# Kernel optimization log

Hardware: AMD Instinct MI355X
Metric: run time of the kernel (lower is better)

Reference implementation:

```python
import jax, jax.numpy as jnp
import numpy as np

N = 12288
D = 256
GAMMA = 0.5
NEG_INF = jnp.float32(-9.0e15)


def setup_inputs() -> dict:
    key = jax.random.key(0)
    k1, k2, k3, k4, k5, k6, k7 = jax.random.split(key, 7)
    h_eu = jax.random.normal(k1, (N, D), dtype=jnp.float32)
    h_po = jax.random.normal(k2, (N, D), dtype=jnp.float32)
    h_lo = jax.random.normal(k3, (N, D), dtype=jnp.float32)
    u = jax.random.uniform(k4, (N, N), dtype=jnp.float32)
    adj = jnp.where(u > 0.9, u, jnp.float32(0.0))
    xav = np.sqrt(2.0) * np.sqrt(6.0 / (D + 1))  # xavier_uniform gain sqrt(2)
    a1 = jax.random.uniform(k5, (D, 1), dtype=jnp.float32, minval=-xav, maxval=xav)
    a2 = jax.random.uniform(k6, (D, 1), dtype=jnp.float32, minval=-xav, maxval=xav)
    a3 = jax.random.uniform(k7, (D, 1), dtype=jnp.float32, minval=-xav, maxval=xav)
    return {"h_eu": h_eu, "h_po": h_po, "h_lo": h_lo, "adj": adj,
            "a1": a1, "a2": a2, "a3": a3}


def reference(h_eu, h_po, h_lo, adj, a1, a2, a3):
    # rank-1 outer-sum score matrix: e[i,j] = <h_eu[i],a1> + <h_po[j],a2> + <h_lo[i],a3>
    e_eu = h_eu @ a1                      # (N,1)
    e_po = (h_po @ a2).T                  # (1,N)
    e_lo = h_lo @ a3                      # (N,1)
    e = jax.nn.leaky_relu(e_eu + e_po + e_lo)  # (N,N), slope 0.01 as in torch
    att = jnp.where(adj > 0, e, NEG_INF)
    att = jax.nn.softmax(att, axis=1)
    # scale each row i by degree (row-sum) of adj row i
    att = att * jnp.sum(adj, axis=1, keepdims=True)
    att = GAMMA * att + (1.0 - GAMMA) * adj
    return att @ h_po                     # (N,D)
```

## Files before the change

kernel.cpp:

```cpp
#include <hip/hip_runtime.h>
#include <hip/hip_bf16.h>


#define NN 12288
#define DD 256
#define BM 48
#define BK 64
#define NSTEPS (NN / BK)
#define BOFF 12288
#define VOFF 45056
#define BUFSZ 45312
#define LOG2E 1.44269504f
#define SHIFT2 36.067376f

typedef __attribute__((ext_vector_type(8))) short s16x8;
typedef __attribute__((ext_vector_type(4))) float f32x4;

__device__ __forceinline__ unsigned short f2bf(float f) {
  unsigned u = __builtin_bit_cast(unsigned, f);
  u += 0x7FFFu + ((u >> 16) & 1u);
  return (unsigned short)(u >> 16);
}
__device__ __forceinline__ unsigned pack_bf2(float a, float b) {
  unsigned short lo = __builtin_bit_cast(unsigned short, __float2bfloat16(a));
  unsigned short hi = __builtin_bit_cast(unsigned short, __float2bfloat16(b));
  return (unsigned)lo | ((unsigned)hi << 16);
}
__device__ __forceinline__ float exp2_hw(float x) {
  float r;
  asm("v_exp_f32 %0, %1" : "=v"(r) : "v"(x));
  return r;
}
__device__ __forceinline__ void gl_lds16(const void* g, void* l) {
  __builtin_amdgcn_global_load_lds(
      (const __attribute__((address_space(1))) void*)g,
      (__attribute__((address_space(3))) void*)l, 16, 0, 0);
}
__device__ __forceinline__ void gl_lds4(const void* g, void* l) {
  __builtin_amdgcn_global_load_lds(
      (const __attribute__((address_space(1))) void*)g,
      (__attribute__((address_space(3))) void*)l, 4, 0, 0);
}

__global__ __launch_bounds__(256) void prep_uv(
    const float* __restrict__ h_eu, const float* __restrict__ h_po,
    const float* __restrict__ h_lo, const float* __restrict__ a1,
    const float* __restrict__ a2, const float* __restrict__ a3,
    float* __restrict__ u, float* __restrict__ v) {
  const int t = threadIdx.x;
  const int wave = t >> 6, lane = t & 63;
  const int r0 = blockIdx.x * 64;
  for (int rr = 0; rr < 16; ++rr) {
    const int row = r0 + wave * 16 + rr;
    const float* pe = h_eu + (size_t)row * DD;
    const float* pl = h_lo + (size_t)row * DD;
    const float* pp = h_po + (size_t)row * DD;
    float su = 0.f, sv = 0.f;
#pragma unroll
    for (int c = 0; c < 4; ++c) {
      const int d = lane + c * 64;
      su = fmaf(pe[d], a1[d], su);
      su = fmaf(pl[d], a3[d], su);
      sv = fmaf(pp[d], a2[d], sv);
    }
#pragma unroll
    for (int m = 32; m; m >>= 1) {
      su += __shfl_xor(su, m, 64);
      sv += __shfl_xor(sv, m, 64);
    }
    if (lane == 0) { u[row] = su * LOG2E; v[row] = sv * LOG2E; }
  }
}

__global__ __launch_bounds__(256) void prep_T(
    const float* __restrict__ hpo, unsigned short* __restrict__ h_poT) {
  const int t = threadIdx.x;
  const int r0 = blockIdx.x * 64;
  unsigned short* dst = h_poT + (size_t)t * NN + r0;
#pragma unroll
  for (int c = 0; c < 16; ++c) {
    unsigned short x0 = f2bf(hpo[(size_t)(r0 + c * 4 + 0) * DD + t]);
    unsigned short x1 = f2bf(hpo[(size_t)(r0 + c * 4 + 1) * DD + t]);
    unsigned short x2 = f2bf(hpo[(size_t)(r0 + c * 4 + 2) * DD + t]);
    unsigned short x3 = f2bf(hpo[(size_t)(r0 + c * 4 + 3) * DD + t]);
    ((uint2*)dst)[c] = make_uint2((unsigned)x0 | ((unsigned)x1 << 16),
                                  (unsigned)x2 | ((unsigned)x3 << 16));
  }
}

__global__ __launch_bounds__(1024) void fused13(
    const float* __restrict__ adj, const float* __restrict__ u2,
    const float* __restrict__ v2, const unsigned short* __restrict__ h_poT,
    float* __restrict__ out) {
  __shared__ __align__(16) char sMem[3 * BUFSZ];
  __shared__ float sq[2][3][16], sa[2][3][16];

  const int t = threadIdx.x;
  const int w = t >> 6, lane = t & 63;
  const int lrow = lane & 15, kgrp = lane >> 4;
  const int i0 = blockIdx.x * BM;

  if (w < 12) {
    const int rg = w >> 2;
    const int dh = (w >> 1) & 1;
    const int kh = w & 1;
    const int row = i0 + rg * 16 + lrow;
    const float u_r = u2[row];
    const float uc1 = u_r - SHIFT2;
    const float uc2 = fmaf(0.01f, u_r, -SHIFT2);
    const int xr = (lrow & 7) << 4;

    const int aOff = (rg * 16 + lrow) * 256;
    const int kA0 = (kh * 128 + kgrp * 32) ^ xr;
    const int kA1 = (kh * 128 + kgrp * 32 + 16) ^ xr;
    const int bOff = BOFF + (dh * 128 + lrow) * 128 + ((kh * 64 + kgrp * 16) ^ xr);
    const int vOff = VOFF + (kh * 32 + kgrp * 8) * 4;

    f32x4 acc1[8] = {};
    f32x4 acc2[8] = {};
    float qsum = 0.f, asum = 0.f;

    __syncthreads();

    int buf = 0;
    for (int s = 0; s < NSTEPS; ++s) {
      const char* bufp = sMem + buf * BUFSZ;
      const f32x4 Vv0 = *(const f32x4*)(bufp + vOff);
      const f32x4 Vv1 = *(const f32x4*)(bufp + vOff + 16);
      const char* ab = bufp + aOff;
      const f32x4 A0 = *(const f32x4*)(ab + kA0);
      const f32x4 A1 = *(const f32x4*)(ab + kA1);
      const float af[8] = {A0[0], A0[1], A0[2], A0[3],
                           A1[0], A1[1], A1[2], A1[3]};
      const float vf[8] = {Vv0[0], Vv0[1], Vv0[2], Vv0[3],
                           Vv1[0], Vv1[1], Vv1[2], Vv1[3]};
      float qv[8];
#pragma unroll
      for (int e = 0; e < 8; ++e) {
        const float t1 = uc1 + vf[e];
        const float t2 = fmaf(0.01f, vf[e], uc2);
        float q = exp2_hw(fmaxf(t1, t2));
        q = (af[e] > 0.f) ? q : 0.f;
        qsum += q; asum += af[e]; qv[e] = q;
      }
      unsigned qp[4], ap[4];
#pragma unroll
      for (int e = 0; e < 4; ++e) {
        qp[e] = pack_bf2(qv[2 * e], qv[2 * e + 1]);
        ap[e] = pack_bf2(af[2 * e], af[2 * e + 1]);
      }
      const s16x8 qa = __builtin_bit_cast(s16x8, *(uint4*)qp);
      const s16x8 aa = __builtin_bit_cast(s16x8, *(uint4*)ap);
      const char* bb = bufp + bOff;
#pragma unroll
      for (int dt = 0; dt < 8; ++dt) {
        const s16x8 b = *(const s16x8*)(bb + dt * 2048);
        acc1[dt] = __builtin_amdgcn_mfma_f32_16x16x32_bf16(qa, b, acc1[dt], 0, 0, 0);
        acc2[dt] = __builtin_amdgcn_mfma_f32_16x16x32_bf16(aa, b, acc2[dt], 0, 0, 0);
      }
      __syncthreads();
      buf = (buf == 2) ? 0 : buf + 1;
    }

    qsum += __shfl_xor(qsum, 16, 64); qsum += __shfl_xor(qsum, 32, 64);
    asum += __shfl_xor(asum, 16, 64); asum += __shfl_xor(asum, 32, 64);
    if (dh == 0 && lane < 16) { sq[kh][rg][lane] = qsum; sa[kh][rg][lane] = asum; }
    __syncthreads();

    f32x4 fin[8];
#pragma unroll
    for (int dt = 0; dt < 8; ++dt) {
#pragma unroll
      for (int g = 0; g < 4; ++g) {
        const int rr = kgrp * 4 + g;
        const float qq = sq[0][rg][rr] + sq[1][rg][rr];
        const float aa2 = sa[0][rg][rr] + sa[1][rg][rr];
        const float cfr = qq > 0.f ? 0.5f * aa2 / qq : 0.f;
        fin[dt][g] = cfr * acc1[dt][g] + 0.5f * acc2[dt][g];
      }
    }
    float* red = (float*)sMem;
    const int rbase = ((rg * 2 + dh) * 8 * 64 + lane) * 4;
    if (kh == 1) {
#pragma unroll
      for (int dt = 0; dt < 8; ++dt) *(f32x4*)&red[rbase + dt * 256] = fin[dt];
    }
    __syncthreads();
    if (kh == 0) {
#pragma unroll
      for (int dt = 0; dt < 8; ++dt) {
        const f32x4 o = *(const f32x4*)&red[rbase + dt * 256];
        const int col = dh * 128 + dt * 16 + lrow;
#pragma unroll
        for (int g = 0; g < 4; ++g)
          out[(size_t)(i0 + rg * 16 + kgrp * 4 + g) * DD + col] = fin[dt][g] + o[g];
      }
    }
  } else {
    const int pid = w - 12;
    const char* pA[3];
    int dA[3];
#pragma unroll
    for (int j = 0; j < 3; ++j) {
      const int idx = pid * 3 + j;
      pA[j] = (const char*)(adj + (size_t)(i0 + idx * 4 + (lane >> 4)) * NN)
              + (((lane & 15) ^ ((idx & 1) * 4 + (lane >> 4))) << 4);
      dA[j] = idx * 1024;
    }
    const int ko = ((lane & 7) ^ (lane >> 3)) << 4;
    const char* pB[8];
    int dB[8];
#pragma unroll
    for (int j = 0; j < 8; ++j) {
      const int ib = pid * 8 + j;
      pB[j] = (const char*)h_poT + (size_t)(ib * 8 + (lane >> 3)) * (NN * 2) + ko;
      dB[j] = BOFF + ib * 1024;
    }
    const float* pV = v2 + lane;

#pragma unroll
    for (int b = 0; b < 2; ++b) {
      char* nb = sMem + b * BUFSZ;
#pragma unroll
      for (int j = 0; j < 3; ++j) { gl_lds16(pA[j], nb + dA[j]); pA[j] += 256; }
#pragma unroll
      for (int j = 0; j < 8; ++j) { gl_lds16(pB[j], nb + dB[j]); pB[j] += 128; }
      gl_lds4(pV, nb + VOFF); pV += 64;
    }
    asm volatile("s_waitcnt vmcnt(12)" ::: "memory");
    __builtin_amdgcn_s_barrier();

    int nbuf = 2;
    for (int s = 0; s < NSTEPS; ++s) {
      if (s < NSTEPS - 2) {
        char* nb = sMem + nbuf * BUFSZ;
#pragma unroll
        for (int j = 0; j < 3; ++j) { gl_lds16(pA[j], nb + dA[j]); pA[j] += 256; }
#pragma unroll
        for (int j = 0; j < 8; ++j) { gl_lds16(pB[j], nb + dB[j]); pB[j] += 128; }
        gl_lds4(pV, nb + VOFF); pV += 64;
        asm volatile("s_waitcnt vmcnt(12)" ::: "memory");
      } else if (s == NSTEPS - 2) {
        asm volatile("s_waitcnt vmcnt(0)" ::: "memory");
      }
      __builtin_amdgcn_s_barrier();
      nbuf = (nbuf == 2) ? 0 : nbuf + 1;
    }
    __syncthreads();
    __syncthreads();
  }
}

__global__ __launch_bounds__(256) void fused_fb(
    const float* __restrict__ adj, const float* __restrict__ u,
    const float* __restrict__ v, const float* __restrict__ hpo,
    float* __restrict__ out) {
#define BMF 32
#define LDA 40
  __shared__ unsigned short qlds[BMF][LDA];
  __shared__ unsigned short alds[BMF][LDA];
  __shared__ unsigned short btf[DD][LDA];
  __shared__ float denom_s[BMF], deg_s[BMF], coef_s[BMF];

  const int t = threadIdx.x;
  const int wave = t >> 6, lane = t & 63;
  const int i0 = blockIdx.x * BMF;
  const int sr = t >> 3;
  const int sc = (t & 7) * 4;
  const float u_r = u[i0 + sr];
  const int d0 = wave * 64;
  const int lrow = lane & 15;
  const int kgrp = lane >> 4;

  f32x4 acc1[2][4] = {};
  f32x4 acc2[2][4] = {};
  float qsum = 0.f, asum = 0.f;

  const float* arow = adj + (size_t)(i0 + sr) * NN + sc;
  float4 a_cur = *(const float4*)(arow);

  constexpr int NSTEP = NN / 32;
  for (int jt = 0; jt < NSTEP; ++jt) {
    const int j = jt * 32;
    float4 a_nxt;
    const bool has_next = (jt + 1 < NSTEP);
    if (has_next) a_nxt = *(const float4*)(arow + j + 32);
    const float4 vv = *(const float4*)(v + j + sc);
    unsigned short qb[4], ab[4];
    {
      const float aa4[4] = {a_cur.x, a_cur.y, a_cur.z, a_cur.w};
      const float vvv[4] = {vv.x, vv.y, vv.z, vv.w};
#pragma unroll
      for (int k = 0; k < 4; ++k) {
        const float a = aa4[k];
        const float s = u_r + vvv[k];
        const float x = fmaxf(s, 0.01f * s);
        const float q = (a > 0.f) ? exp2_hw(x - SHIFT2) : 0.f;
        qsum += q;
        asum += a;
        qb[k] = f2bf(q);
        ab[k] = f2bf(a);
      }
    }
    *(uint2*)&qlds[sr][sc] = make_uint2((unsigned)qb[0] | ((unsigned)qb[1] << 16),
                                        (unsigned)qb[2] | ((unsigned)qb[3] << 16));
    *(uint2*)&alds[sr][sc] = make_uint2((unsigned)ab[0] | ((unsigned)ab[1] << 16),
                                        (unsigned)ab[2] | ((unsigned)ab[3] << 16));
    {
      const int br = t >> 3;
      const float* src = hpo + (size_t)(j + br) * DD;
#pragma unroll
      for (int cc = 0; cc < 8; ++cc) {
        const int c = (t & 7) * 4 + cc * 32;
        const float4 hv = *(const float4*)(src + c);
        btf[c + 0][br] = f2bf(hv.x);
        btf[c + 1][br] = f2bf(hv.y);
        btf[c + 2][br] = f2bf(hv.z);
        btf[c + 3][br] = f2bf(hv.w);
      }
    }
    __syncthreads();

    const s16x8 qa0 = *(const s16x8*)&qlds[lrow][kgrp * 8];
    const s16x8 qa1 = *(const s16x8*)&qlds[16 + lrow][kgrp * 8];
    const s16x8 ad0 = *(const s16x8*)&alds[lrow][kgrp * 8];
    const s16x8 ad1 = *(const s16x8*)&alds[16 + lrow][kgrp * 8];
#pragma unroll
    for (int dt = 0; dt < 4; ++dt) {
      const s16x8 b = *(const s16x8*)&btf[d0 + dt * 16 + lrow][kgrp * 8];
      acc1[0][dt] = __builtin_amdgcn_mfma_f32_16x16x32_bf16(qa0, b, acc1[0][dt], 0, 0, 0);
      acc1[1][dt] = __builtin_amdgcn_mfma_f32_16x16x32_bf16(qa1, b, acc1[1][dt], 0, 0, 0);
      acc2[0][dt] = __builtin_amdgcn_mfma_f32_16x16x32_bf16(ad0, b, acc2[0][dt], 0, 0, 0);
      acc2[1][dt] = __builtin_amdgcn_mfma_f32_16x16x32_bf16(ad1, b, acc2[1][dt], 0, 0, 0);
    }
    __syncthreads();
    if (has_next) a_cur = a_nxt;
  }
#pragma unroll
  for (int m = 1; m <= 4; m <<= 1) {
    qsum += __shfl_xor(qsum, m, 64);
    asum += __shfl_xor(asum, m, 64);
  }
  if ((t & 7) == 0) { denom_s[sr] = qsum; deg_s[sr] = asum; }
  __syncthreads();
  if (t < BMF) {
    const float dn = denom_s[t];
    coef_s[t] = dn > 0.f ? 0.5f * deg_s[t] / dn : 0.f;
  }
  __syncthreads();
#pragma unroll
  for (int f = 0; f < 2; ++f) {
#pragma unroll
    for (int dt = 0; dt < 4; ++dt) {
      const int col = d0 + dt * 16 + lrow;
#pragma unroll
      for (int g = 0; g < 4; ++g) {
        const int r = f * 16 + kgrp * 4 + g;
        out[(size_t)(i0 + r) * DD + col] =
            coef_s[r] * acc1[f][dt][g] + 0.5f * acc2[f][dt][g];
      }
    }
  }
}

extern "C" void kernel_launch(void* const* d_in, const int* in_sizes, int n_in,
                              void* d_out, int out_size, void* d_ws, size_t ws_size,
                              hipStream_t stream) {
  const float* h_eu = (const float*)d_in[0];
  const float* h_po = (const float*)d_in[1];
  const float* h_lo = (const float*)d_in[2];
  const float* adj  = (const float*)d_in[3];
  const float* a1   = (const float*)d_in[4];
  const float* a2   = (const float*)d_in[5];
  const float* a3   = (const float*)d_in[6];
  float* out = (float*)d_out;

  const size_t need_full = (size_t)2 * NN * 4 + (size_t)NN * DD * 2;
  float* u = (float*)d_ws;
  float* v = u + NN;
  unsigned short* h_poT = (unsigned short*)(v + NN);
  const bool big_ws = ws_size >= need_full;

  prep_uv<<<NN / 64, 256, 0, stream>>>(h_eu, h_po, h_lo, a1, a2, a3, u, v);
  if (big_ws) {
    prep_T<<<NN / 64, 256, 0, stream>>>(h_po, h_poT);
    fused13<<<NN / BM, 1024, 0, stream>>>(adj, u, v, h_poT, out);
  } else {
    fused_fb<<<NN / 32, 256, 0, stream>>>(adj, u, v, h_po, out);
  }
}
```

Before: 253.3 us.

## Load h_poT B-operand directly from global into registers instead of LDS staging

Compute warps now read the transposed bf16 h_po tile straight from global memory into registers each k-step, and the producer warps only stage adjacency and v into shared memory. This shrinks the per-stage LDS buffer and removes LDS write/read traffic for B. In exchange, B is fetched redundantly by the three row-group warps and without software prefetch, so global/L2 latency lands directly in the MFMA loop.

Result: slower. 667.4 us (+163.5%).

```diff
diff --git a/kernel.cpp b/kernel.cpp
--- a/kernel.cpp
+++ b/kernel.cpp
@@ -7,9 +7,8 @@
 #define BM 48
 #define BK 64
 #define NSTEPS (NN / BK)
-#define BOFF 12288
-#define VOFF 45056
-#define BUFSZ 45312
+#define VOFF 12288
+#define BUFSZ 12544
 #define LOG2E 1.44269504f
 #define SHIFT2 36.067376f
 
@@ -88,11 +87,11 @@
   }
 }
 
-__global__ __launch_bounds__(1024) void fused13(
+__global__ __launch_bounds__(1024) void fused14(
     const float* __restrict__ adj, const float* __restrict__ u2,
     const float* __restrict__ v2, const unsigned short* __restrict__ h_poT,
     float* __restrict__ out) {
-  __shared__ __align__(16) char sMem[3 * BUFSZ];
+  __shared__ __align__(16) char sMem[49152];
   __shared__ float sq[2][3][16], sa[2][3][16];
 
   const int t = threadIdx.x;
@@ -113,8 +112,13 @@
     const int aOff = (rg * 16 + lrow) * 256;
     const int kA0 = (kh * 128 + kgrp * 32) ^ xr;
     const int kA1 = (kh * 128 + kgrp * 32 + 16) ^ xr;
-    const int bOff = BOFF + (dh * 128 + lrow) * 128 + ((kh * 64 + kgrp * 16) ^ xr);
     const int vOff = VOFF + (kh * 32 + kgrp * 8) * 4;
+
+    const char* bbase[8];
+#pragma unroll
+    for (int dt = 0; dt < 8; ++dt)
+      bbase[dt] = (const char*)h_poT + (size_t)(dh * 128 + dt * 16) * (NN * 2);
+    unsigned boff = (unsigned)(lrow * NN + kh * 32 + kgrp * 8) * 2;
 
     f32x4 acc1[8] = {};
     f32x4 acc2[8] = {};
@@ -124,6 +128,12 @@
 
     int buf = 0;
     for (int s = 0; s < NSTEPS; ++s) {
+      uint4 b[8];
+#pragma unroll
+      for (int dt = 0; dt < 8; ++dt)
+        b[dt] = *(const uint4*)(bbase[dt] + boff);
+      boff += 128;
+
       const char* bufp = sMem + buf * BUFSZ;
       const f32x4 Vv0 = *(const f32x4*)(bufp + vOff);
       const f32x4 Vv1 = *(const f32x4*)(bufp + vOff + 16);
@@ -151,12 +161,11 @@
       }
       const s16x8 qa = __builtin_bit_cast(s16x8, *(uint4*)qp);
       const s16x8 aa = __builtin_bit_cast(s16x8, *(uint4*)ap);
-      const char* bb = bufp + bOff;
 #pragma unroll
       for (int dt = 0; dt < 8; ++dt) {
-        const s16x8 b = *(const s16x8*)(bb + dt * 2048);
-        acc1[dt] = __builtin_amdgcn_mfma_f32_16x16x32_bf16(qa, b, acc1[dt], 0, 0, 0);
-        acc2[dt] = __builtin_amdgcn_mfma_f32_16x16x32_bf16(aa, b, acc2[dt], 0, 0, 0);
+        const s16x8 bb = __builtin_bit_cast(s16x8, b[dt]);
+        acc1[dt] = __builtin_amdgcn_mfma_f32_16x16x32_bf16(qa, bb, acc1[dt], 0, 0, 0);
+        acc2[dt] = __builtin_amdgcn_mfma_f32_16x16x32_bf16(aa, bb, acc2[dt], 0, 0, 0);
       }
       __syncthreads();
       buf = (buf == 2) ? 0 : buf + 1;
@@ -207,15 +216,6 @@
               + (((lane & 15) ^ ((idx & 1) * 4 + (lane >> 4))) << 4);
       dA[j] = idx * 1024;
     }
-    const int ko = ((lane & 7) ^ (lane >> 3)) << 4;
-    const char* pB[8];
-    int dB[8];
-#pragma unroll
-    for (int j = 0; j < 8; ++j) {
-      const int ib = pid * 8 + j;
-      pB[j] = (const char*)h_poT + (size_t)(ib * 8 + (lane >> 3)) * (NN * 2) + ko;
-      dB[j] = BOFF + ib * 1024;
-    }
     const float* pV = v2 + lane;
 
 #pragma unroll
@@ -223,11 +223,9 @@
       char* nb = sMem + b * BUFSZ;
 #pragma unroll
       for (int j = 0; j < 3; ++j) { gl_lds16(pA[j], nb + dA[j]); pA[j] += 256; }
-#pragma unroll
-      for (int j = 0; j < 8; ++j) { gl_lds16(pB[j], nb + dB[j]); pB[j] += 128; }
       gl_lds4(pV, nb + VOFF); pV += 64;
     }
-    asm volatile("s_waitcnt vmcnt(12)" ::: "memory");
+    asm volatile("s_waitcnt vmcnt(4)" ::: "memory");
     __builtin_amdgcn_s_barrier();
 
     int nbuf = 2;
@@ -236,10 +234,8 @@
         char* nb = sMem + nbuf * BUFSZ;
 #pragma unroll
         for (int j = 0; j < 3; ++j) { gl_lds16(pA[j], nb + dA[j]); pA[j] += 256; }
-#pragma unroll
-        for (int j = 0; j < 8; ++j) { gl_lds16(pB[j], nb + dB[j]); pB[j] += 128; }
         gl_lds4(pV, nb + VOFF); pV += 64;
-        asm volatile("s_waitcnt vmcnt(12)" ::: "memory");
+        asm volatile("s_waitcnt vmcnt(4)" ::: "memory");
       } else if (s == NSTEPS - 2) {
         asm volatile("s_waitcnt vmcnt(0)" ::: "memory");
       }
@@ -384,7 +380,7 @@
   prep_uv<<<NN / 64, 256, 0, stream>>>(h_eu, h_po, h_lo, a1, a2, a3, u, v);
   if (big_ws) {
     prep_T<<<NN / 64, 256, 0, stream>>>(h_po, h_poT);
-    fused13<<<NN / BM, 1024, 0, stream>>>(adj, u, v, h_poT, out);
+    fused14<<<NN / BM, 1024, 0, stream>>>(adj, u, v, h_poT, out);
   } else {
     fused_fb<<<NN / 32, 256, 0, stream>>>(adj, u, v, h_po, out);
   }
```

## Cut compute waves to four, each covering three row groups, two blocks per CU

Applied to the files above, without the earlier changes.

Compute warps drop from 12 to 4. Each one now handles all three 16-row groups, so every B fragment loaded from LDS feeds three times as many MFMAs and B reads from LDS fall. The block shrinks from 1024 to 512 threads with launch bounds (512,2), aiming for two resident blocks per CU. The cost is six times the accumulator registers per compute thread (48 f32x4 instead of 16). That risks spilling, and with fewer compute waves there is less latency hiding for the exp and packing work.

New measurement: 522.2 us. +106.2%, slower.

```diff
diff --git a/kernel.cpp b/kernel.cpp
--- a/kernel.cpp
+++ b/kernel.cpp
@@ -88,7 +88,7 @@
   }
 }
 
-__global__ __launch_bounds__(1024) void fused13(
+__global__ __launch_bounds__(512, 2) void fused15(
     const float* __restrict__ adj, const float* __restrict__ u2,
     const float* __restrict__ v2, const unsigned short* __restrict__ h_poT,
     float* __restrict__ out) {
@@ -100,25 +100,28 @@
   const int lrow = lane & 15, kgrp = lane >> 4;
   const int i0 = blockIdx.x * BM;
 
-  if (w < 12) {
-    const int rg = w >> 2;
-    const int dh = (w >> 1) & 1;
+  if (w < 4) {
+    const int dh = w >> 1;
     const int kh = w & 1;
-    const int row = i0 + rg * 16 + lrow;
-    const float u_r = u2[row];
-    const float uc1 = u_r - SHIFT2;
-    const float uc2 = fmaf(0.01f, u_r, -SHIFT2);
     const int xr = (lrow & 7) << 4;
 
-    const int aOff = (rg * 16 + lrow) * 256;
+    float uc1[3], uc2[3];
+#pragma unroll
+    for (int m = 0; m < 3; ++m) {
+      const float ur = u2[i0 + m * 16 + lrow];
+      uc1[m] = ur - SHIFT2;
+      uc2[m] = fmaf(0.01f, ur, -SHIFT2);
+    }
+
+    const int aOff0 = lrow * 256;
     const int kA0 = (kh * 128 + kgrp * 32) ^ xr;
     const int kA1 = (kh * 128 + kgrp * 32 + 16) ^ xr;
     const int bOff = BOFF + (dh * 128 + lrow) * 128 + ((kh * 64 + kgrp * 16) ^ xr);
     const int vOff = VOFF + (kh * 32 + kgrp * 8) * 4;
 
-    f32x4 acc1[8] = {};
-    f32x4 acc2[8] = {};
-    float qsum = 0.f, asum = 0.f;
+    f32x4 acc1[3][8] = {};
+    f32x4 acc2[3][8] = {};
+    float qsum[3] = {0.f, 0.f, 0.f}, asum[3] = {0.f, 0.f, 0.f};
 
     __syncthreads();
 
@@ -127,77 +130,107 @@
       const char* bufp = sMem + buf * BUFSZ;
       const f32x4 Vv0 = *(const f32x4*)(bufp + vOff);
       const f32x4 Vv1 = *(const f32x4*)(bufp + vOff + 16);
-      const char* ab = bufp + aOff;
-      const f32x4 A0 = *(const f32x4*)(ab + kA0);
-      const f32x4 A1 = *(const f32x4*)(ab + kA1);
-      const float af[8] = {A0[0], A0[1], A0[2], A0[3],
-                           A1[0], A1[1], A1[2], A1[3]};
       const float vf[8] = {Vv0[0], Vv0[1], Vv0[2], Vv0[3],
                            Vv1[0], Vv1[1], Vv1[2], Vv1[3]};
-      float qv[8];
-#pragma unroll
-      for (int e = 0; e < 8; ++e) {
-        const float t1 = uc1 + vf[e];
-        const float t2 = fmaf(0.01f, vf[e], uc2);
-        float q = exp2_hw(fmaxf(t1, t2));
-        q = (af[e] > 0.f) ? q : 0.f;
-        qsum += q; asum += af[e]; qv[e] = q;
-      }
-      unsigned qp[4], ap[4];
-#pragma unroll
-      for (int e = 0; e < 4; ++e) {
-        qp[e] = pack_bf2(qv[2 * e], qv[2 * e + 1]);
-        ap[e] = pack_bf2(af[2 * e], af[2 * e + 1]);
-      }
-      const s16x8 qa = __builtin_bit_cast(s16x8, *(uint4*)qp);
-      const s16x8 aa = __builtin_bit_cast(s16x8, *(uint4*)ap);
+
+      s16x8 qa[3], aa[3];
+#pragma unroll
+      for (int m = 0; m < 3; ++m) {
+        const char* ab = bufp + aOff0 + m * 4096;
+        const f32x4 A0 = *(const f32x4*)(ab + kA0);
+        const f32x4 A1 = *(const f32x4*)(ab + kA1);
+        const float af[8] = {A0[0], A0[1], A0[2], A0[3],
+                             A1[0], A1[1], A1[2], A1[3]};
+        float qv[8];
+#pragma unroll
+        for (int e = 0; e < 8; ++e) {
+          const float t1 = uc1[m] + vf[e];
+          const float t2 = fmaf(0.01f, vf[e], uc2[m]);
+          float q = exp2_hw(fmaxf(t1, t2));
+          q = (af[e] > 0.f) ? q : 0.f;
+          qsum[m] += q; asum[m] += af[e]; qv[e] = q;
+        }
+        unsigned qp[4], ap[4];
+#pragma unroll
+        for (int e = 0; e < 4; ++e) {
+          qp[e] = pack_bf2(qv[2 * e], qv[2 * e + 1]);
+          ap[e] = pack_bf2(af[2 * e], af[2 * e + 1]);
+        }
+        qa[m] = __builtin_bit_cast(s16x8, *(uint4*)qp);
+        aa[m] = __builtin_bit_cast(s16x8, *(uint4*)ap);
+      }
+
       const char* bb = bufp + bOff;
 #pragma unroll
       for (int dt = 0; dt < 8; ++dt) {
         const s16x8 b = *(const s16x8*)(bb + dt * 2048);
-        acc1[dt] = __builtin_amdgcn_mfma_f32_16x16x32_bf16(qa, b, acc1[dt], 0, 0, 0);
-        acc2[dt] = __builtin_amdgcn_mfma_f32_16x16x32_bf16(aa, b, acc2[dt], 0, 0, 0);
+#pragma unroll
+        for (int m = 0; m < 3; ++m) {
+          acc1[m][dt] = __builtin_amdgcn_mfma_f32_16x16x32_bf16(qa[m], b, acc1[m][dt], 0, 0, 0);
+          acc2[m][dt] = __builtin_amdgcn_mfma_f32_16x16x32_bf16(aa[m], b, acc2[m][dt], 0, 0, 0);
+        }
       }
       __syncthreads();
       buf = (buf == 2) ? 0 : buf + 1;
     }
 
-    qsum += __shfl_xor(qsum, 16, 64); qsum += __shfl_xor(qsum, 32, 64);
-    asum += __shfl_xor(asum, 16, 64); asum += __shfl_xor(asum, 32, 64);
-    if (dh == 0 && lane < 16) { sq[kh][rg][lane] = qsum; sa[kh][rg][lane] = asum; }
-    __syncthreads();
-
-    f32x4 fin[8];
-#pragma unroll
-    for (int dt = 0; dt < 8; ++dt) {
-#pragma unroll
-      for (int g = 0; g < 4; ++g) {
-        const int rr = kgrp * 4 + g;
-        const float qq = sq[0][rg][rr] + sq[1][rg][rr];
-        const float aa2 = sa[0][rg][rr] + sa[1][rg][rr];
-        const float cfr = qq > 0.f ? 0.5f * aa2 / qq : 0.f;
-        fin[dt][g] = cfr * acc1[dt][g] + 0.5f * acc2[dt][g];
-      }
-    }
+#pragma unroll
+    for (int m = 0; m < 3; ++m) {
+      qsum[m] += __shfl_xor(qsum[m], 16, 64);
+      qsum[m] += __shfl_xor(qsum[m], 32, 64);
+      asum[m] += __shfl_xor(asum[m], 16, 64);
+      asum[m] += __shfl_xor(asum[m], 32, 64);
+    }
+    if (dh == 0 && lane < 16) {
+#pragma unroll
+      for (int m = 0; m < 3; ++m) {
+        sq[kh][m][lane] = qsum[m];
+        sa[kh][m][lane] = asum[m];
+      }
+    }
+    __syncthreads();
+
     float* red = (float*)sMem;
-    const int rbase = ((rg * 2 + dh) * 8 * 64 + lane) * 4;
     if (kh == 1) {
 #pragma unroll
-      for (int dt = 0; dt < 8; ++dt) *(f32x4*)&red[rbase + dt * 256] = fin[dt];
+      for (int m = 0; m < 3; ++m) {
+#pragma unroll
+        for (int dt = 0; dt < 8; ++dt) {
+          f32x4 fin;
+#pragma unroll
+          for (int g = 0; g < 4; ++g) {
+            const int rr = kgrp * 4 + g;
+            const float qq = sq[0][m][rr] + sq[1][m][rr];
+            const float aa2 = sa[0][m][rr] + sa[1][m][rr];
+            const float cfr = qq > 0.f ? 0.5f * aa2 / qq : 0.f;
+            fin[g] = cfr * acc1[m][dt][g] + 0.5f * acc2[m][dt][g];
+          }
+          *(f32x4*)&red[(((dh * 3 + m) * 8 + dt) * 64 + lane) * 4] = fin;
+        }
+      }
     }
     __syncthreads();
     if (kh == 0) {
 #pragma unroll
-      for (int dt = 0; dt < 8; ++dt) {
-        const f32x4 o = *(const f32x4*)&red[rbase + dt * 256];
-        const int col = dh * 128 + dt * 16 + lrow;
-#pragma unroll
-        for (int g = 0; g < 4; ++g)
-          out[(size_t)(i0 + rg * 16 + kgrp * 4 + g) * DD + col] = fin[dt][g] + o[g];
+      for (int m = 0; m < 3; ++m) {
+#pragma unroll
+        for (int dt = 0; dt < 8; ++dt) {
+          const f32x4 o = *(const f32x4*)&red[(((dh * 3 + m) * 8 + dt) * 64 + lane) * 4];
+          const int col = dh * 128 + dt * 16 + lrow;
+#pragma unroll
+          for (int g = 0; g < 4; ++g) {
+            const int rr = kgrp * 4 + g;
+            const float qq = sq[0][m][rr] + sq[1][m][rr];
+            const float aa2 = sa[0][m][rr] + sa[1][m][rr];
+            const float cfr = qq > 0.f ? 0.5f * aa2 / qq : 0.f;
+            out[(size_t)(i0 + m * 16 + rr) * DD + col] =
+                cfr * acc1[m][dt][g] + 0.5f * acc2[m][dt][g] + o[g];
+          }
+        }
       }
     }
   } else {
-    const int pid = w - 12;
+    const int pid = w - 4;
     const char* pA[3];
     int dA[3];
 #pragma unroll
@@ -384,7 +417,7 @@
   prep_uv<<<NN / 64, 256, 0, stream>>>(h_eu, h_po, h_lo, a1, a2, a3, u, v);
   if (big_ws) {
     prep_T<<<NN / 64, 256, 0, stream>>>(h_po, h_poT);
-    fused13<<<NN / BM, 1024, 0, stream>>>(adj, u, v, h_poT, out);
+    fused15<<<NN / BM, 512, 0, stream>>>(adj, u, v, h_poT, out);
   } else {
     fused_fb<<<NN / 32, 256, 0, stream>>>(adj, u, v, h_po, out);
   }
```

## Split producer warps into separate adj and h_po pipelines with deeper adj buffering

Applied to the files above, without the earlier changes.

Replaces the shared triple-buffered stage holding adj, h_poT and v with separate LDS rings. Adjacency and v use a 4-deep ring loaded by two warps, and h_poT uses a 3-deep ring loaded by two other warps, each with its own vmcnt waits. The aim is to keep more adjacency loads in flight, since adj is the dominant HBM stream, and to keep the two streams from stalling each other. LDS use rises slightly to about 148KB, and the waitcnt tail logic grows more complex.

Measured after the change: 249.7 us. Within noise of the previous version (-1.4%).

```diff
diff --git a/kernel.cpp b/kernel.cpp
--- a/kernel.cpp
+++ b/kernel.cpp
@@ -7,9 +7,9 @@
 #define BM 48
 #define BK 64
 #define NSTEPS (NN / BK)
-#define BOFF 12288
-#define VOFF 45056
-#define BUFSZ 45312
+#define ABUFSZ 12544
+#define AVOFF 12288
+#define BBUFSZ 32768
 #define LOG2E 1.44269504f
 #define SHIFT2 36.067376f
 
@@ -88,11 +88,12 @@
   }
 }
 
-__global__ __launch_bounds__(1024) void fused13(
+__global__ __launch_bounds__(1024) void fused18(
     const float* __restrict__ adj, const float* __restrict__ u2,
     const float* __restrict__ v2, const unsigned short* __restrict__ h_poT,
     float* __restrict__ out) {
-  __shared__ __align__(16) char sMem[3 * BUFSZ];
+  __shared__ __align__(16) char sAdjM[4 * ABUFSZ];
+  __shared__ __align__(16) char sBM[3 * BBUFSZ];
   __shared__ float sq[2][3][16], sa[2][3][16];
 
   const int t = threadIdx.x;
@@ -113,8 +114,8 @@
     const int aOff = (rg * 16 + lrow) * 256;
     const int kA0 = (kh * 128 + kgrp * 32) ^ xr;
     const int kA1 = (kh * 128 + kgrp * 32 + 16) ^ xr;
-    const int bOff = BOFF + (dh * 128 + lrow) * 128 + ((kh * 64 + kgrp * 16) ^ xr);
-    const int vOff = VOFF + (kh * 32 + kgrp * 8) * 4;
+    const int bOff = (dh * 128 + lrow) * 128 + ((kh * 64 + kgrp * 16) ^ xr);
+    const int vOff = AVOFF + (kh * 32 + kgrp * 8) * 4;
 
     f32x4 acc1[8] = {};
     f32x4 acc2[8] = {};
@@ -122,14 +123,15 @@
 
     __syncthreads();
 
-    int buf = 0;
+    int ab = 0, bb = 0;
     for (int s = 0; s < NSTEPS; ++s) {
-      const char* bufp = sMem + buf * BUFSZ;
-      const f32x4 Vv0 = *(const f32x4*)(bufp + vOff);
-      const f32x4 Vv1 = *(const f32x4*)(bufp + vOff + 16);
-      const char* ab = bufp + aOff;
-      const f32x4 A0 = *(const f32x4*)(ab + kA0);
-      const f32x4 A1 = *(const f32x4*)(ab + kA1);
+      const char* abufp = sAdjM + ab * ABUFSZ;
+      const char* bbufp = sBM + bb * BBUFSZ;
+      const f32x4 Vv0 = *(const f32x4*)(abufp + vOff);
+      const f32x4 Vv1 = *(const f32x4*)(abufp + vOff + 16);
+      const char* abp = abufp + aOff;
+      const f32x4 A0 = *(const f32x4*)(abp + kA0);
+      const f32x4 A1 = *(const f32x4*)(abp + kA1);
       const float af[8] = {A0[0], A0[1], A0[2], A0[3],
                            A1[0], A1[1], A1[2], A1[3]};
       const float vf[8] = {Vv0[0], Vv0[1], Vv0[2], Vv0[3],
@@ -151,15 +153,15 @@
       }
       const s16x8 qa = __builtin_bit_cast(s16x8, *(uint4*)qp);
       const s16x8 aa = __builtin_bit_cast(s16x8, *(uint4*)ap);
-      const char* bb = bufp + bOff;
 #pragma unroll
       for (int dt = 0; dt < 8; ++dt) {
-        const s16x8 b = *(const s16x8*)(bb + dt * 2048);
+        const s16x8 b = *(const s16x8*)(bbufp + bOff + dt * 2048);
         acc1[dt] = __builtin_amdgcn_mfma_f32_16x16x32_bf16(qa, b, acc1[dt], 0, 0, 0);
         acc2[dt] = __builtin_amdgcn_mfma_f32_16x16x32_bf16(aa, b, acc2[dt], 0, 0, 0);
       }
       __syncthreads();
-      buf = (buf == 2) ? 0 : buf + 1;
+      ab = (ab == 3) ? 0 : ab + 1;
+      bb = (bb == 2) ? 0 : bb + 1;
     }
 
     qsum += __shfl_xor(qsum, 16, 64); qsum += __shfl_xor(qsum, 32, 64);
@@ -179,7 +181,7 @@
         fin[dt][g] = cfr * acc1[dt][g] + 0.5f * acc2[dt][g];
       }
     }
-    float* red = (float*)sMem;
+    float* red = (float*)sBM;
     const int rbase = ((rg * 2 + dh) * 8 * 64 + lane) * 4;
     if (kh == 1) {
 #pragma unroll
@@ -196,55 +198,80 @@
           out[(size_t)(i0 + rg * 16 + kgrp * 4 + g) * DD + col] = fin[dt][g] + o[g];
       }
     }
-  } else {
+  } else if (w < 14) {
     const int pid = w - 12;
-    const char* pA[3];
-    int dA[3];
-#pragma unroll
-    for (int j = 0; j < 3; ++j) {
-      const int idx = pid * 3 + j;
+    const char* pA[6];
+    int dA[6];
+#pragma unroll
+    for (int j = 0; j < 6; ++j) {
+      const int idx = pid * 6 + j;
       pA[j] = (const char*)(adj + (size_t)(i0 + idx * 4 + (lane >> 4)) * NN)
               + (((lane & 15) ^ ((idx & 1) * 4 + (lane >> 4))) << 4);
       dA[j] = idx * 1024;
     }
-    const int ko = ((lane & 7) ^ (lane >> 3)) << 4;
-    const char* pB[8];
-    int dB[8];
-#pragma unroll
-    for (int j = 0; j < 8; ++j) {
-      const int ib = pid * 8 + j;
-      pB[j] = (const char*)h_poT + (size_t)(ib * 8 + (lane >> 3)) * (NN * 2) + ko;
-      dB[j] = BOFF + ib * 1024;
-    }
     const float* pV = v2 + lane;
 
 #pragma unroll
-    for (int b = 0; b < 2; ++b) {
-      char* nb = sMem + b * BUFSZ;
-#pragma unroll
-      for (int j = 0; j < 3; ++j) { gl_lds16(pA[j], nb + dA[j]); pA[j] += 256; }
-#pragma unroll
-      for (int j = 0; j < 8; ++j) { gl_lds16(pB[j], nb + dB[j]); pB[j] += 128; }
-      gl_lds4(pV, nb + VOFF); pV += 64;
-    }
-    asm volatile("s_waitcnt vmcnt(12)" ::: "memory");
+    for (int b = 0; b < 3; ++b) {
+      char* nb = sAdjM + b * ABUFSZ;
+#pragma unroll
+      for (int j = 0; j < 6; ++j) { gl_lds16(pA[j], nb + dA[j]); pA[j] += 256; }
+      gl_lds4(pV, nb + AVOFF); pV += 64;
+    }
+    asm volatile("s_waitcnt vmcnt(14)" ::: "memory");
     __builtin_amdgcn_s_barrier();
 
-    int nbuf = 2;
+    int nb = 3;
     for (int s = 0; s < NSTEPS; ++s) {
-      if (s < NSTEPS - 2) {
-        char* nb = sMem + nbuf * BUFSZ;
-#pragma unroll
-        for (int j = 0; j < 3; ++j) { gl_lds16(pA[j], nb + dA[j]); pA[j] += 256; }
-#pragma unroll
-        for (int j = 0; j < 8; ++j) { gl_lds16(pB[j], nb + dB[j]); pB[j] += 128; }
-        gl_lds4(pV, nb + VOFF); pV += 64;
-        asm volatile("s_waitcnt vmcnt(12)" ::: "memory");
+      if (s <= NSTEPS - 4) {
+        char* nbuf = sAdjM + nb * ABUFSZ;
+#pragma unroll
+        for (int j = 0; j < 6; ++j) { gl_lds16(pA[j], nbuf + dA[j]); pA[j] += 256; }
+        gl_lds4(pV, nbuf + AVOFF); pV += 64;
+        asm volatile("s_waitcnt vmcnt(14)" ::: "memory");
+      } else if (s == NSTEPS - 3) {
+        asm volatile("s_waitcnt vmcnt(7)" ::: "memory");
       } else if (s == NSTEPS - 2) {
         asm volatile("s_waitcnt vmcnt(0)" ::: "memory");
       }
       __builtin_amdgcn_s_barrier();
-      nbuf = (nbuf == 2) ? 0 : nbuf + 1;
+      nb = (nb == 3) ? 0 : nb + 1;
+    }
+    __syncthreads();
+    __syncthreads();
+  } else {
+    const int pid = w - 14;
+    const int ko = ((lane & 7) ^ (lane >> 3)) << 4;
+    const char* pB[16];
+    int dB[16];
+#pragma unroll
+    for (int j = 0; j < 16; ++j) {
+      const int ib = pid * 16 + j;
+      pB[j] = (const char*)h_poT + (size_t)(ib * 8 + (lane >> 3)) * (NN * 2) + ko;
+      dB[j] = ib * 1024;
+    }
+
+#pragma unroll
+    for (int b = 0; b < 2; ++b) {
+      char* nbuf = sBM + b * BBUFSZ;
+#pragma unroll
+      for (int j = 0; j < 16; ++j) { gl_lds16(pB[j], nbuf + dB[j]); pB[j] += 128; }
+    }
+    asm volatile("s_waitcnt vmcnt(16)" ::: "memory");
+    __builtin_amdgcn_s_barrier();
+
+    int nb = 2;
+    for (int s = 0; s < NSTEPS; ++s) {
+      if (s <= NSTEPS - 3) {
+        char* nbuf = sBM + nb * BBUFSZ;
+#pragma unroll
+        for (int j = 0; j < 16; ++j) { gl_lds16(pB[j], nbuf + dB[j]); pB[j] += 128; }
+        asm volatile("s_waitcnt vmcnt(16)" ::: "memory");
+      } else if (s == NSTEPS - 2) {
+        asm volatile("s_waitcnt vmcnt(0)" ::: "memory");
+      }
+      __builtin_amdgcn_s_barrier();
+      nb = (nb == 2) ? 0 : nb + 1;
     }
     __syncthreads();
     __syncthreads();
@@ -384,7 +411,7 @@
   prep_uv<<<NN / 64, 256, 0, stream>>>(h_eu, h_po, h_lo, a1, a2, a3, u, v);
   if (big_ws) {
     prep_T<<<NN / 64, 256, 0, stream>>>(h_po, h_poT);
-    fused13<<<NN / BM, 1024, 0, stream>>>(adj, u, v, h_poT, out);
+    fused18<<<NN / BM, 1024, 0, stream>>>(adj, u, v, h_poT, out);
   } else {
     fused_fb<<<NN / 32, 256, 0, stream>>>(adj, u, v, h_po, out);
   }
```
